# Performance work log

Measured on AMD Instinct MI355X. Metric: run time of the kernel, lower is better.

## Reference

```python
import jax, jax.numpy as jnp
import numpy as np

HEADS = 16
PHI = (1.0 + np.sqrt(5.0)) / 2.0


def setup_inputs() -> dict:
    key = jax.random.key(0)
    k1, k2, k3, k4 = jax.random.split(key, 4)
    B, L, D = 2, 2048, 1024
    x = jax.random.normal(k1, (B, L, D), dtype=jnp.float32)
    # nn.Linear(dim, 3*dim, bias=False): store as [D, 3D] for x @ W
    w_qkv = jax.random.normal(k2, (D, 3 * D), dtype=jnp.float32) * (D ** -0.5)
    w_proj = jax.random.normal(k3, (D, D), dtype=jnp.float32) * (D ** -0.5)
    b_proj = jax.random.normal(k4, (D,), dtype=jnp.float32) * 0.01
    return {"x": x, "w_qkv": w_qkv, "w_proj": w_proj, "b_proj": b_proj}


def phi_bias(L):
    # pos[i] = (i * phi) mod 1 ; bias = log(exp(-|pos_i - pos_j|) + 1e-8)
    pos = (jnp.arange(L, dtype=jnp.float32) * PHI) % 1.0
    dist = jnp.abs(pos[:, None] - pos[None, :])  # [L, L]
    return jnp.log(jnp.exp(-dist) + 1e-8)


def reference(x, w_qkv, w_proj, b_proj):
    B, L, D = x.shape
    H = HEADS
    Dh = D // H
    scale = Dh ** -0.5
    qkv = (x @ w_qkv).reshape(B, L, 3, H, Dh)
    q = jnp.transpose(qkv[:, :, 0], (0, 2, 1, 3))  # [B, H, L, Dh]
    k = jnp.transpose(qkv[:, :, 1], (0, 2, 1, 3))
    v = jnp.transpose(qkv[:, :, 2], (0, 2, 1, 3))
    attn = jnp.einsum("bhid,bhjd->bhij", q, k) * scale  # [B, H, L, L]
    attn = attn + phi_bias(L)[None, None]  # additive phi-distance bias
    attn = jax.nn.softmax(attn, axis=-1)
    out = jnp.einsum("bhij,bhjd->bhid", attn, v)  # [B, H, L, Dh]
    out = jnp.transpose(out, (0, 2, 1, 3)).reshape(B, L, D)
    return out @ w_proj + b_proj
```

## Files before the change

kernel.cpp:

```cpp
#include <hip/hip_runtime.h>
#include <math.h>


typedef _Float16 f16;
typedef _Float16 f16x4 __attribute__((ext_vector_type(4)));
typedef _Float16 f16x8 __attribute__((ext_vector_type(8)));
typedef float f32x4 __attribute__((ext_vector_type(4)));

#define MFMA32(a, b, c) __builtin_amdgcn_mfma_f32_16x16x32_f16(a, b, c, 0, 0, 0)

static constexpr int Bsz = 2, Lseq = 2048, Dm = 1024, H = 16, Dh = 64;
static constexpr int Mtot = Bsz * Lseq;
static constexpr int NQKV = 3 * Dm;
static constexpr float PHI_F = 1.61803398874989484820f;
static constexpr float LOG2E = 1.44269504088896f;
static constexpr float QS = 0.125f * LOG2E;
static constexpr float CSTEP = 0.55417527999932633f;

__device__ __forceinline__ void load16_to_lds(const f16* g, f16* l) {
  __builtin_amdgcn_global_load_lds(
      (const __attribute__((address_space(1))) unsigned int*)g,
      (__attribute__((address_space(3))) unsigned int*)l, 16, 0, 0);
}

__device__ __forceinline__ void barrier_fenced() {
  __builtin_amdgcn_sched_barrier(0);
  __builtin_amdgcn_s_barrier();
  __builtin_amdgcn_sched_barrier(0);
}

__global__ __launch_bounds__(256) void cast_f32_f16(const float* __restrict__ in,
                                                    f16* __restrict__ out, int n) {
  int i = (blockIdx.x * 256 + threadIdx.x) * 4;
  if (i < n) {
    float4 v = *reinterpret_cast<const float4*>(in + i);
    f16 t[4] = {(f16)v.x, (f16)v.y, (f16)v.z, (f16)v.w};
    *reinterpret_cast<uint2*>(out + i) = *reinterpret_cast<uint2*>(t);
  }
}

__global__ __launch_bounds__(256) void transpose_cast(const float* __restrict__ in,
                                                      f16* __restrict__ out,
                                                      int K, int N) {
  __shared__ float tile[32][33];
  int n0 = blockIdx.x * 32, k0 = blockIdx.y * 32;
  int tx = threadIdx.x & 31, ty = threadIdx.x >> 5;
#pragma unroll
  for (int r = 0; r < 32; r += 8)
    tile[ty + r][tx] = in[(size_t)(k0 + ty + r) * N + n0 + tx];
  __syncthreads();
#pragma unroll
  for (int r = 0; r < 32; r += 8)
    out[(size_t)(n0 + ty + r) * K + k0 + tx] = (f16)tile[tx][ty + r];
}

__global__ __launch_bounds__(256) void v_transpose(const f16* __restrict__ in,
                                                   f16* __restrict__ out) {
  __shared__ f16 td[64][68];
  int bh = blockIdx.y, l0 = blockIdx.x * 64;
  int tid = threadIdx.x;
  const f16* src = in + (size_t)bh * Lseq * Dh;
#pragma unroll
  for (int c = tid; c < 512; c += 256) {
    int row = c >> 3, col = (c & 7) * 8;
    uint4 v = *reinterpret_cast<const uint4*>(src + (size_t)(l0 + row) * Dh + col);
    f16 tmp[8];
    *reinterpret_cast<uint4*>(tmp) = v;
#pragma unroll
    for (int j = 0; j < 8; j++) td[col + j][row] = tmp[j];
  }
  __syncthreads();
  f16* dst = out + (size_t)bh * Dh * Lseq;
#pragma unroll
  for (int c = tid; c < 512; c += 256) {
    int d = c >> 3, co = c & 7;
    int jh = co >> 2, qd = co & 3;
    f16 tmp[8];
#pragma unroll
    for (int e = 0; e < 4; e++) tmp[e] = td[d][jh * 32 + qd * 4 + e];
#pragma unroll
    for (int e = 0; e < 4; e++) tmp[4 + e] = td[d][jh * 32 + 16 + qd * 4 + e];
    *reinterpret_cast<uint4*>(dst + (size_t)d * Lseq + l0 + co * 8) =
        *reinterpret_cast<uint4*>(tmp);
  }
}

template <int MODE>
__global__ __launch_bounds__(256) void gemm_f16(
    const f16* __restrict__ A, const f16* __restrict__ Bt,
    int M, int N, int K,
    f16* __restrict__ qb, f16* __restrict__ kb, f16* __restrict__ vl,
    float* __restrict__ out, const float* __restrict__ bias) {
  constexpr int BM = (MODE == 0) ? 128 : 64;
  constexpr int MI = BM / 32;
  constexpr int AI = BM / 32;
  __shared__ f16 As[BM * 64];
  __shared__ f16 Bs[128 * 64];

  int tid = threadIdx.x;
  int wave = tid >> 6, lane = tid & 63;
  int quad = lane >> 4, l16 = lane & 15;
  int wm = (wave >> 1) * (MI * 16), wn = (wave & 1) * 64;

  int lid = blockIdx.x;
  int xcd = lid & 7, t = lid >> 3;
  int m0, n0;
  if (MODE == 0) {
    int mg = xcd >> 1, ng = xcd & 1;
    m0 = (mg * 8 + t / 12) * 128;
    n0 = (ng * 12 + t % 12) * 128;
  } else {
    m0 = (xcd * 8 + (t >> 3)) * 64;
    n0 = (t & 7) * 128;
  }

  const int gu = (lane & 7) ^ (lane >> 3);
  const f16* gA[AI];
  f16* lA[AI];
#pragma unroll
  for (int i = 0; i < AI; i++) {
    int it = wave * AI + i;
    gA[i] = A + (size_t)(m0 + it * 8 + (lane >> 3)) * K + gu * 8;
    lA[i] = As + it * 512;
  }
  const f16* gB[4];
  f16* lB[4];
#pragma unroll
  for (int i = 0; i < 4; i++) {
    int it = wave * 4 + i;
    gB[i] = Bt + (size_t)(n0 + it * 8 + (lane >> 3)) * K + gu * 8;
    lB[i] = Bs + it * 512;
  }

  f32x4 acc[MI][4] = {};

  for (int k0 = 0; k0 < K; k0 += 64) {
#pragma unroll
    for (int i = 0; i < AI; i++) load16_to_lds(gA[i] + k0, lA[i]);
#pragma unroll
    for (int i = 0; i < 4; i++) load16_to_lds(gB[i] + k0, lB[i]);
    __syncthreads();
#pragma unroll
    for (int s = 0; s < 2; s++) {
      f16x8 a[MI], b[4];
#pragma unroll
      for (int i = 0; i < MI; i++) {
        int row = wm + i * 16 + l16;
        a[i] = *reinterpret_cast<const f16x8*>(
            As + row * 64 + (((s * 4 + quad) ^ (l16 & 7)) * 8));
      }
#pragma unroll
      for (int j = 0; j < 4; j++) {
        int row = wn + j * 16 + l16;
        b[j] = *reinterpret_cast<const f16x8*>(
            Bs + row * 64 + (((s * 4 + quad) ^ (l16 & 7)) * 8));
      }
#pragma unroll
      for (int i = 0; i < MI; i++)
#pragma unroll
        for (int j = 0; j < 4; j++)
          acc[i][j] = MFMA32(a[i], b[j], acc[i][j]);
    }
    __syncthreads();
  }

#pragma unroll
  for (int i = 0; i < MI; i++) {
#pragma unroll
    for (int j = 0; j < 4; j++) {
      int n = n0 + wn + j * 16 + l16;
#pragma unroll
      for (int r = 0; r < 4; r++) {
        int m = m0 + wm + i * 16 + quad * 4 + r;
        if (MODE == 0) {
          int ty = n >> 10;
          int df = n & 1023;
          int h = df >> 6, dh = df & 63;
          int b = m >> 11, l = m & 2047;
          size_t idx = (((size_t)(b * H + h)) * Lseq + l) * Dh + dh;
          if (ty == 0)
            qb[idx] = (f16)(acc[i][j][r] * QS);
          else if (ty == 1)
            kb[idx] = (f16)acc[i][j][r];
          else
            vl[idx] = (f16)acc[i][j][r];
        } else {
          out[(size_t)m * N + n] = acc[i][j][r] + bias[n];
        }
      }
    }
  }
}

__global__ __launch_bounds__(256, 4) void attn_kernel(
    const f16* __restrict__ qb,
    const f16* __restrict__ kb,
    const f16* __restrict__ vb,
    f16* __restrict__ ctx) {
  __shared__ __align__(16) unsigned char smem[32768];
  f16* Ks = (f16*)smem;
  f16* Vs = (f16*)(smem + 16384);

  int bh = blockIdx.y;
  int q0 = blockIdx.x * 64;
  int tid = threadIdx.x, wave = tid >> 6, lane = tid & 63;
  int quad = lane >> 4, l16 = lane & 15;
  int jhalf = wave >> 1, qhalf = wave & 1;

  f16x8 qfrag[2][2];
  float pq[2];
#pragma unroll
  for (int set = 0; set < 2; set++) {
    int q = q0 + qhalf * 32 + set * 16 + l16;
    const f16* Qrow = qb + ((size_t)bh * Lseq + q) * Dh;
    qfrag[set][0] = *reinterpret_cast<const f16x8*>(Qrow + quad * 8);
    qfrag[set][1] = *reinterpret_cast<const f16x8*>(Qrow + 32 + quad * 8);
    pq[set] = fmodf((float)q * PHI_F, 1.0f);
  }

  float pk[2][4];
#pragma unroll
  for (int jb = 0; jb < 2; jb++)
#pragma unroll
    for (int r = 0; r < 4; r++) {
      int j = jhalf * 32 + jb * 16 + quad * 4 + r;
      pk[jb][r] = fmodf((float)j * PHI_F, 1.0f);
    }

  const f16* Kbh = kb + (size_t)bh * Lseq * Dh;
  const f16* Vbh = vb + (size_t)bh * Dh * Lseq;
  const int gu = (lane & 7) ^ (lane >> 3);
  const f16* gK[2];
  const f16* gV[2];
  f16* lK[2];
  f16* lV[2];
#pragma unroll
  for (int i = 0; i < 2; i++) {
    int g8 = (wave * 2 + i) * 8 + (lane >> 3);
    gK[i] = Kbh + (size_t)g8 * Dh + gu * 8;
    gV[i] = Vbh + (size_t)g8 * Lseq + gu * 8;
    lK[i] = Ks + (wave * 2 + i) * 512;
    lV[i] = Vs + (wave * 2 + i) * 512;
  }

  const f16 one = (f16)1.0f;
  const f16x8 ones8 = {one, one, one, one, one, one, one, one};

  f32x4 acc_o[2][4] = {};
  f32x4 acc_l[2] = {};

  auto stage = [&](int buf, int j0) __attribute__((always_inline)) {
#pragma unroll
    for (int i = 0; i < 2; i++) {
      load16_to_lds(gK[i] + (size_t)j0 * Dh, lK[i] + buf * 4096);
      load16_to_lds(gV[i] + j0, lV[i] + buf * 4096);
    }
  };

  auto compute = [&](int buf) __attribute__((always_inline)) {
    const f16* Kc = Ks + buf * 4096;
    const f16* Vc = Vs + buf * 4096;

    f32x4 accs[2][2] = {};
    __builtin_amdgcn_s_setprio(1);
#pragma unroll
    for (int s = 0; s < 2; s++)
#pragma unroll
      for (int jb = 0; jb < 2; jb++) {
        f16x8 kf = *reinterpret_cast<const f16x8*>(
            Kc + (jhalf * 32 + jb * 16 + l16) * 64 +
            (((s * 4 + quad) ^ (l16 & 7)) * 8));
        accs[0][jb] = MFMA32(kf, qfrag[0][s], accs[0][jb]);
        accs[1][jb] = MFMA32(kf, qfrag[1][s], accs[1][jb]);
      }
    __builtin_amdgcn_s_setprio(0);

    f16x8 pf8[2];
#pragma unroll
    for (int set = 0; set < 2; set++) {
#pragma unroll
      for (int jb = 0; jb < 2; jb++) {
        float p[4];
#pragma unroll
        for (int r = 0; r < 4; r++) {
          float d = pq[set] - pk[jb][r];
          float arg = fmaf(-LOG2E, fabsf(d), accs[set][jb][r]);
          p[r] = __builtin_amdgcn_exp2f(arg);
        }
        auto lo = __builtin_amdgcn_cvt_pkrtz(p[0], p[1]);
        auto hi = __builtin_amdgcn_cvt_pkrtz(p[2], p[3]);
        pf8[set][jb * 4 + 0] = lo[0];
        pf8[set][jb * 4 + 1] = lo[1];
        pf8[set][jb * 4 + 2] = hi[0];
        pf8[set][jb * 4 + 3] = hi[1];
      }
      acc_l[set] = MFMA32(ones8, pf8[set], acc_l[set]);
    }
#pragma unroll
    for (int jb = 0; jb < 2; jb++)
#pragma unroll
      for (int r = 0; r < 4; r++)
        pk[jb][r] = __builtin_amdgcn_fractf(pk[jb][r] + CSTEP);

    __builtin_amdgcn_s_setprio(1);
#pragma unroll
    for (int dblk = 0; dblk < 4; dblk++) {
      int row = dblk * 16 + l16;
      f16x8 va = *reinterpret_cast<const f16x8*>(
          Vc + row * 64 + (((jhalf * 4 + quad) ^ (l16 & 7)) * 8));
      acc_o[0][dblk] = MFMA32(va, pf8[0], acc_o[0][dblk]);
      acc_o[1][dblk] = MFMA32(va, pf8[1], acc_o[1][dblk]);
    }
    __builtin_amdgcn_s_setprio(0);
  };

  stage(0, 0);
#pragma unroll 1
  for (int j0 = 0; j0 < Lseq; j0 += 128) {
    stage(1, j0 + 64);
    asm volatile("s_waitcnt vmcnt(4)" ::: "memory");
    barrier_fenced();
    compute(0);
    barrier_fenced();
    int jn = (j0 + 128 < Lseq) ? j0 + 128 : 0;
    stage(0, jn);
    asm volatile("s_waitcnt vmcnt(4)" ::: "memory");
    barrier_fenced();
    compute(1);
    barrier_fenced();
  }
  asm volatile("s_waitcnt vmcnt(0)" ::: "memory");
  barrier_fenced();

  float* Oex = (float*)smem;
  float* Lex = (float*)(smem + 16384);
  if (jhalf == 1) {
#pragma unroll
    for (int set = 0; set < 2; set++) {
#pragma unroll
      for (int dblk = 0; dblk < 4; dblk++)
#pragma unroll
        for (int r = 0; r < 4; r++)
          Oex[(((qhalf * 2 + set) * 4 + dblk) * 16 + quad * 4 + r) * 16 + l16] =
              acc_o[set][dblk][r];
      if (quad == 0) Lex[(qhalf * 2 + set) * 16 + l16] = acc_l[set][0];
    }
  }
  __syncthreads();
  if (jhalf == 0) {
    int b = bh >> 4, h = bh & 15;
#pragma unroll
    for (int set = 0; set < 2; set++) {
      float ltot = acc_l[set][0] + Lex[(qhalf * 2 + set) * 16 + l16];
      float inv = 1.0f / ltot;
      int q = q0 + qhalf * 32 + set * 16 + l16;
      f16* crow = ctx + (size_t)(b * Lseq + q) * Dm + h * 64;
#pragma unroll
      for (int dblk = 0; dblk < 4; dblk++) {
        f16x4 o;
#pragma unroll
        for (int r = 0; r < 4; r++) {
          float full = acc_o[set][dblk][r] +
              Oex[(((qhalf * 2 + set) * 4 + dblk) * 16 + quad * 4 + r) * 16 + l16];
          o[r] = (f16)(full * inv);
        }
        *reinterpret_cast<uint2*>(crow + dblk * 16 + quad * 4) =
            *reinterpret_cast<uint2*>(&o);
      }
    }
  }
}

extern "C" void kernel_launch(void* const* d_in, const int* in_sizes, int n_in,
                              void* d_out, int out_size, void* d_ws, size_t ws_size,
                              hipStream_t stream) {
  const float* x      = (const float*)d_in[0];
  const float* w_qkv  = (const float*)d_in[1];
  const float* w_proj = (const float*)d_in[2];
  const float* b_proj = (const float*)d_in[3];
  float* out = (float*)d_out;

  f16* xb    = (f16*)d_ws;
  f16* wqkvT = xb + (size_t)Mtot * Dm;
  f16* wpT   = wqkvT + (size_t)NQKV * Dm;
  f16* qb    = wpT + (size_t)Dm * Dm;
  f16* kb    = qb + (size_t)Bsz * H * Lseq * Dh;
  f16* vb    = kb + (size_t)Bsz * H * Lseq * Dh;
  f16* ctx   = vb + (size_t)Bsz * H * Lseq * Dh;
  f16* vl    = ctx;

  cast_f32_f16<<<(Mtot * Dm) / (256 * 4), 256, 0, stream>>>(x, xb, Mtot * Dm);
  transpose_cast<<<dim3(NQKV / 32, Dm / 32), 256, 0, stream>>>(w_qkv, wqkvT, Dm, NQKV);
  transpose_cast<<<dim3(Dm / 32, Dm / 32), 256, 0, stream>>>(w_proj, wpT, Dm, Dm);

  gemm_f16<0><<<768, 256, 0, stream>>>(
      xb, wqkvT, Mtot, NQKV, Dm, qb, kb, vl, nullptr, nullptr);

  v_transpose<<<dim3(Lseq / 64, Bsz * H), 256, 0, stream>>>(vl, vb);

  attn_kernel<<<dim3(Lseq / 64, Bsz * H), 256, 0, stream>>>(qb, kb, vb, ctx);

  gemm_f16<1><<<512, 256, 0, stream>>>(
      ctx, wpT, Mtot, Dm, Dm, nullptr, nullptr, nullptr, out, b_proj);
}
```

Baseline: 190.6 us.

## Software-pipeline attention loop with split K/V staging and cross-tile overlap

Splits K and V staging into separate async LDS loads and restructures the loop so QK^T of the next tile overlaps with PV of the previous tile. This cuts barriers per iteration from four to three. The phi bias is now written into the accumulator as its initial value, which removes the per-element bias FMA during softmax, and the LDS fragment pointers are computed once before the loop. The cost is higher register pressure from holding two tiles' accumulators and probabilities at once, plus tighter vmcnt accounting that must stay correct.

```diff
diff --git a/kernel.cpp b/kernel.cpp
--- a/kernel.cpp
+++ b/kernel.cpp
@@ -249,44 +249,62 @@
   f32x4 acc_o[2][4] = {};
   f32x4 acc_l[2] = {};
 
-  auto stage = [&](int buf, int j0) __attribute__((always_inline)) {
-#pragma unroll
-    for (int i = 0; i < 2; i++) {
-      load16_to_lds(gK[i] + (size_t)j0 * Dh, lK[i] + buf * 4096);
-      load16_to_lds(gV[i] + j0, lV[i] + buf * 4096);
-    }
-  };
-
-  auto compute = [&](int buf) __attribute__((always_inline)) {
-    const f16* Kc = Ks + buf * 4096;
-    const f16* Vc = Vs + buf * 4096;
-
-    f32x4 accs[2][2] = {};
+  const f16* kfp[2][2];
+#pragma unroll
+  for (int s = 0; s < 2; s++)
+#pragma unroll
+    for (int jb = 0; jb < 2; jb++)
+      kfp[s][jb] = Ks + (jhalf * 32 + jb * 16 + l16) * 64 +
+                   (((s * 4 + quad) ^ (l16 & 7)) * 8);
+  const f16* vfp[4];
+#pragma unroll
+  for (int dblk = 0; dblk < 4; dblk++)
+    vfp[dblk] = Vs + (dblk * 16 + l16) * 64 +
+                (((jhalf * 4 + quad) ^ (l16 & 7)) * 8);
+
+  auto stageK = [&](int buf, int j0) __attribute__((always_inline)) {
+    load16_to_lds(gK[0] + (size_t)j0 * Dh, lK[0] + buf * 4096);
+    load16_to_lds(gK[1] + (size_t)j0 * Dh, lK[1] + buf * 4096);
+  };
+  auto stageV = [&](int buf, int j0) __attribute__((always_inline)) {
+    load16_to_lds(gV[0] + j0, lV[0] + buf * 4096);
+    load16_to_lds(gV[1] + j0, lV[1] + buf * 4096);
+  };
+
+  auto initbias = [&](f32x4 a[2][2], const float pkt[2][4])
+      __attribute__((always_inline)) {
+#pragma unroll
+    for (int set = 0; set < 2; set++)
+#pragma unroll
+      for (int jb = 0; jb < 2; jb++)
+#pragma unroll
+        for (int r = 0; r < 4; r++)
+          a[set][jb][r] = -LOG2E * fabsf(pq[set] - pkt[jb][r]);
+  };
+
+  auto qk = [&](int buf, f32x4 a[2][2]) __attribute__((always_inline)) {
     __builtin_amdgcn_s_setprio(1);
 #pragma unroll
     for (int s = 0; s < 2; s++)
 #pragma unroll
       for (int jb = 0; jb < 2; jb++) {
-        f16x8 kf = *reinterpret_cast<const f16x8*>(
-            Kc + (jhalf * 32 + jb * 16 + l16) * 64 +
-            (((s * 4 + quad) ^ (l16 & 7)) * 8));
-        accs[0][jb] = MFMA32(kf, qfrag[0][s], accs[0][jb]);
-        accs[1][jb] = MFMA32(kf, qfrag[1][s], accs[1][jb]);
+        f16x8 kf = *reinterpret_cast<const f16x8*>(kfp[s][jb] + buf * 4096);
+        a[0][jb] = MFMA32(kf, qfrag[0][s], a[0][jb]);
+        a[1][jb] = MFMA32(kf, qfrag[1][s], a[1][jb]);
       }
     __builtin_amdgcn_s_setprio(0);
-
-    f16x8 pf8[2];
+  };
+
+  auto smfin = [&](const f32x4 a[2][2], f16x8 pf8[2])
+      __attribute__((always_inline)) {
 #pragma unroll
     for (int set = 0; set < 2; set++) {
 #pragma unroll
       for (int jb = 0; jb < 2; jb++) {
         float p[4];
 #pragma unroll
-        for (int r = 0; r < 4; r++) {
-          float d = pq[set] - pk[jb][r];
-          float arg = fmaf(-LOG2E, fabsf(d), accs[set][jb][r]);
-          p[r] = __builtin_amdgcn_exp2f(arg);
-        }
+        for (int r = 0; r < 4; r++)
+          p[r] = __builtin_amdgcn_exp2f(a[set][jb][r]);
         auto lo = __builtin_amdgcn_cvt_pkrtz(p[0], p[1]);
         auto hi = __builtin_amdgcn_cvt_pkrtz(p[2], p[3]);
         pf8[set][jb * 4 + 0] = lo[0];
@@ -296,38 +314,63 @@
       }
       acc_l[set] = MFMA32(ones8, pf8[set], acc_l[set]);
     }
-#pragma unroll
-    for (int jb = 0; jb < 2; jb++)
-#pragma unroll
-      for (int r = 0; r < 4; r++)
-        pk[jb][r] = __builtin_amdgcn_fractf(pk[jb][r] + CSTEP);
-
-    __builtin_amdgcn_s_setprio(1);
+  };
+
+  auto pv = [&](int buf, const f16x8 pf8[2]) __attribute__((always_inline)) {
 #pragma unroll
     for (int dblk = 0; dblk < 4; dblk++) {
-      int row = dblk * 16 + l16;
-      f16x8 va = *reinterpret_cast<const f16x8*>(
-          Vc + row * 64 + (((jhalf * 4 + quad) ^ (l16 & 7)) * 8));
+      f16x8 va = *reinterpret_cast<const f16x8*>(vfp[dblk] + buf * 4096);
       acc_o[0][dblk] = MFMA32(va, pf8[0], acc_o[0][dblk]);
       acc_o[1][dblk] = MFMA32(va, pf8[1], acc_o[1][dblk]);
     }
-    __builtin_amdgcn_s_setprio(0);
-  };
-
-  stage(0, 0);
+  };
+
+  stageK(0, 0);
+  stageV(0, 0);
+  stageK(1, 64);
+
 #pragma unroll 1
   for (int j0 = 0; j0 < Lseq; j0 += 128) {
-    stage(1, j0 + 64);
-    asm volatile("s_waitcnt vmcnt(4)" ::: "memory");
+    asm volatile("s_waitcnt vmcnt(2)" ::: "memory");
     barrier_fenced();
-    compute(0);
+    stageV(1, j0 + 64);
+
+    f32x4 accs0[2][2];
+    initbias(accs0, pk);
+    qk(0, accs0);
+    float pk1[2][4];
+#pragma unroll
+    for (int jb = 0; jb < 2; jb++)
+#pragma unroll
+      for (int r = 0; r < 4; r++)
+        pk1[jb][r] = __builtin_amdgcn_fractf(pk[jb][r] + CSTEP);
+    f16x8 pf80[2];
+    smfin(accs0, pf80);
+
+    asm volatile("s_waitcnt vmcnt(2)" ::: "memory");
     barrier_fenced();
-    int jn = (j0 + 128 < Lseq) ? j0 + 128 : 0;
-    stage(0, jn);
-    asm volatile("s_waitcnt vmcnt(4)" ::: "memory");
+    stageK(0, (j0 + 128) & (Lseq - 1));
+
+    f32x4 accs1[2][2];
+    initbias(accs1, pk1);
+    qk(1, accs1);
+    pv(0, pf80);
+    f16x8 pf81[2];
+    smfin(accs1, pf81);
+#pragma unroll
+    for (int jb = 0; jb < 2; jb++)
+#pragma unroll
+      for (int r = 0; r < 4; r++)
+        pk[jb][r] = __builtin_amdgcn_fractf(pk1[jb][r] + CSTEP);
+
+    asm volatile("s_waitcnt vmcnt(2)" ::: "memory");
     barrier_fenced();
-    compute(1);
-    barrier_fenced();
+    stageV(0, (j0 + 128) & (Lseq - 1));
+    stageK(1, (j0 + 192) & (Lseq - 1));
+
+    __builtin_amdgcn_s_setprio(1);
+    pv(1, pf81);
+    __builtin_amdgcn_s_setprio(0);
   }
   asm volatile("s_waitcnt vmcnt(0)" ::: "memory");
   barrier_fenced();
```

New measurement: 192.2 us. Within noise of the previous version (+0.9%).
